# Kernel tuning notes

Measured on AMD Instinct MI355X. Metric: run time of the kernel, lower is better.

The kernel has to match this reference:

```python
import jax, jax.numpy as jnp
import numpy as np

B, T, D = 2, 2048, 512
HEADS, DIM_HEAD, MAX_LAG = 8, 64, 5
INNER = HEADS * DIM_HEAD


def setup_inputs() -> dict:
    key = jax.random.key(0)
    k0, k1, k2, k3, k4 = jax.random.split(key, 5)
    x = jax.random.normal(k0, (B, T, D), dtype=jnp.float32)
    # Linear weights stored as (in, out); torch applies x @ W.T with W (out, in).
    Wq = jax.random.normal(k1, (D, INNER), dtype=jnp.float32) * (1.0 / np.sqrt(D))
    Wk = jax.random.normal(k2, (D, INNER), dtype=jnp.float32) * (1.0 / np.sqrt(D))
    Wv = jax.random.normal(k3, (D, INNER), dtype=jnp.float32) * (1.0 / np.sqrt(D))
    Wo = jax.random.normal(k4, (INNER, D), dtype=jnp.float32) * (1.0 / np.sqrt(INNER))
    bo = jnp.zeros((D,), dtype=jnp.float32)
    # Module's init: lag_weights = log(exp(-lags/(max_lag/3))) = -lags/(max_lag/3)
    lags = jnp.arange(MAX_LAG + 1, dtype=jnp.float32)
    lag_weights = jnp.broadcast_to(-(lags / (MAX_LAG / 3.0)), (HEADS, MAX_LAG + 1)).astype(jnp.float32)
    return {"x": x, "Wq": Wq, "Wk": Wk, "Wv": Wv, "Wo": Wo, "bo": bo, "lag_weights": lag_weights}


def reference(x, Wq, Wk, Wv, Wo, bo, lag_weights):
    b, t, _ = x.shape
    h, dh = HEADS, DIM_HEAD
    scale = dh ** -0.5
    # context defaults to x (self-attention)
    q = (x @ Wq).reshape(b, t, h, dh).transpose(0, 2, 1, 3)  # b h t d
    k = (x @ Wk).reshape(b, t, h, dh).transpose(0, 2, 1, 3)
    v = (x @ Wv).reshape(b, t, h, dh).transpose(0, 2, 1, 3)
    sim = jnp.einsum('bhid,bhjd->bhij', q, k) * scale  # b h t t
    # causal mask: keep j <= i
    causal = jnp.tril(jnp.ones((t, t), dtype=bool))
    neg = -jnp.finfo(sim.dtype).max
    sim = jnp.where(causal[None, None], sim, neg)
    # learned additive time-lag bias: lag_adj[h,i,j] = softmax(lag_weights)[h, clamp(i-j,0,MAX_LAG)]
    ti = jnp.arange(t)
    time_lags = jnp.clip(ti[:, None] - ti[None, :], 0, MAX_LAG)  # t t
    lag_probs = jax.nn.softmax(lag_weights, axis=-1)  # h (L+1)
    lag_adj = lag_probs[:, time_lags]  # h t t
    sim = sim + lag_adj[None]
    attn = jax.nn.softmax(sim, axis=-1)
    out = jnp.einsum('bhij,bhjd->bhid', attn, v)
    out = out.transpose(0, 2, 1, 3).reshape(b, t, h * dh)  # b t inner
    return out @ Wo + bo  # dropout is identity at eval
```

## Files before the change

kernel.cpp:

```cpp
#include <hip/hip_runtime.h>
#include <hip/hip_bf16.h>

#define BB 2
#define TT 2048
#define DD 512
#define HH 8
#define DH 64
#define INNER 512
#define MAXLAG 5

typedef __attribute__((ext_vector_type(8))) short short8;
typedef __attribute__((ext_vector_type(4))) float floatx4;
typedef unsigned short ushort_t;

__device__ inline unsigned short f2bf(float f) {
    unsigned u = __float_as_uint(f);
    unsigned r = (u + 0x7FFFu + ((u >> 16) & 1u)) >> 16;
    return (unsigned short)r;
}
__device__ inline float bf2f(unsigned short u) {
    return __uint_as_float(((unsigned)u) << 16);
}

#define NXE (BB * TT * DD)

__global__ __launch_bounds__(256)
void cvt_kernel(const float* __restrict__ x,
                const float* __restrict__ wq, const float* __restrict__ wk,
                const float* __restrict__ wv, const float* __restrict__ wo,
                ushort_t* __restrict__ xb,
                ushort_t* __restrict__ wqt, ushort_t* __restrict__ wkt,
                ushort_t* __restrict__ wvt, ushort_t* __restrict__ wot)
{
    __shared__ float T[32][33];
    const int bid = blockIdx.x;
    if (bid < 1024) {
        int off = (bid * 256 + threadIdx.x) * 8;
        float4 a = *(const float4*)&x[off];
        float4 b = *(const float4*)&x[off + 4];
        ushort_t t[8];
        t[0] = f2bf(a.x); t[1] = f2bf(a.y); t[2] = f2bf(a.z); t[3] = f2bf(a.w);
        t[4] = f2bf(b.x); t[5] = f2bf(b.y); t[6] = f2bf(b.z); t[7] = f2bf(b.w);
        *(uint4*)&xb[off] = *(const uint4*)t;
        return;
    }
    const int r = bid - 1024;
    const int z = r >> 8;
    const int tile = r & 255;
    const float* s = (z == 0) ? wq : (z == 1) ? wk : (z == 2) ? wv : wo;
    ushort_t*    d = (z == 0) ? wqt : (z == 1) ? wkt : (z == 2) ? wvt : wot;
    const int k0 = (tile & 15) * 32;
    const int n0 = (tile >> 4) * 32;
    {
        const int kk = threadIdx.x >> 3;
        const int n4 = (threadIdx.x & 7) * 4;
        float4 v = *(const float4*)&s[(size_t)(k0 + kk) * 512 + n0 + n4];
        T[kk][n4 + 0] = v.x; T[kk][n4 + 1] = v.y;
        T[kk][n4 + 2] = v.z; T[kk][n4 + 3] = v.w;
    }
    __syncthreads();
    {
        const int nn = threadIdx.x >> 3;
        const int k4 = (threadIdx.x & 7) * 4;
        ushort4 o;
        o.x = f2bf(T[k4 + 0][nn]); o.y = f2bf(T[k4 + 1][nn]);
        o.z = f2bf(T[k4 + 2][nn]); o.w = f2bf(T[k4 + 3][nn]);
        *(ushort4*)&d[(size_t)(n0 + nn) * 512 + k0 + k4] = o;
    }
}

#define GM 64
#define GN 64
#define GK 32

template <typename OutT>
__global__ __launch_bounds__(256)
void gemm64(const ushort_t* __restrict__ A,
            const ushort_t* __restrict__ B0, const ushort_t* __restrict__ B1,
            const ushort_t* __restrict__ B2,
            OutT* __restrict__ O0, OutT* __restrict__ O1, OutT* __restrict__ O2,
            const float* __restrict__ bias, int M, int N, int K, int vtrans)
{
    const ushort_t* Bw = (blockIdx.z == 0) ? B0 : ((blockIdx.z == 1) ? B1 : B2);
    OutT*           O  = (blockIdx.z == 0) ? O0 : ((blockIdx.z == 1) ? O1 : O2);
    const int dotrans = vtrans && (blockIdx.z == 2);

    __shared__ ushort_t As[GM * GK];
    __shared__ ushort_t Bs[GN * GK];

    const int tid  = threadIdx.x;
    const int wave = tid >> 6;
    const int lane = tid & 63;
    const int quad = lane >> 4;
    const int l15  = lane & 15;
    const int wr   = wave >> 1;
    const int wc   = wave & 1;
    const int bm   = blockIdx.y * GM;
    const int bn   = blockIdx.x * GN;

    const ushort_t* ap = &A[(size_t)(bm + (tid >> 2)) * K + (tid & 3) * 8];
    const ushort_t* bp = &Bw[(size_t)(bn + (tid >> 2)) * K + (tid & 3) * 8];

    floatx4 acc[2][2];
#pragma unroll
    for (int i = 0; i < 2; ++i)
#pragma unroll
        for (int j = 0; j < 2; ++j) acc[i][j] = (floatx4){0.f, 0.f, 0.f, 0.f};

    uint4 pa = *(const uint4*)ap;
    uint4 pb = *(const uint4*)bp;

    for (int k0 = 0; k0 < K; k0 += GK) {
        __syncthreads();
        *(uint4*)&As[tid * 8] = pa;
        *(uint4*)&Bs[tid * 8] = pb;
        if (k0 + GK < K) {
            pa = *(const uint4*)(ap + k0 + GK);
            pb = *(const uint4*)(bp + k0 + GK);
        }
        __syncthreads();

        short8 af[2], bf[2];
#pragma unroll
        for (int mt = 0; mt < 2; ++mt)
            af[mt] = *(const short8*)&As[(((wr * 32 + mt * 16 + l15) << 2) + quad) * 8];
#pragma unroll
        for (int nt = 0; nt < 2; ++nt)
            bf[nt] = *(const short8*)&Bs[(((wc * 32 + nt * 16 + l15) << 2) + quad) * 8];
#pragma unroll
        for (int mt = 0; mt < 2; ++mt)
#pragma unroll
            for (int nt = 0; nt < 2; ++nt)
                acc[mt][nt] = __builtin_amdgcn_mfma_f32_16x16x32_bf16(
                    af[mt], bf[nt], acc[mt][nt], 0, 0, 0);
    }

    if (dotrans) {
#pragma unroll
        for (int mt = 0; mt < 2; ++mt) {
            const int m0 = bm + wr * 32 + mt * 16 + quad * 4;
            const int b  = m0 >> 11;
            const int t0 = m0 & 2047;
#pragma unroll
            for (int nt = 0; nt < 2; ++nt) {
                const int n = bn + wc * 32 + nt * 16 + l15;
                const int h = n >> 6, dd = n & 63;
                ushort4 o;
                o.x = f2bf(acc[mt][nt][0]); o.y = f2bf(acc[mt][nt][1]);
                o.z = f2bf(acc[mt][nt][2]); o.w = f2bf(acc[mt][nt][3]);
                *(ushort4*)&((ushort_t*)O)[((size_t)((b * 8 + h) * 64 + dd)) * 2048 + t0] = o;
            }
        }
        return;
    }

    float bv[2] = {0.f, 0.f};
    if (bias) {
#pragma unroll
        for (int nt = 0; nt < 2; ++nt)
            bv[nt] = bias[bn + wc * 32 + nt * 16 + l15];
    }
#pragma unroll
    for (int mt = 0; mt < 2; ++mt) {
#pragma unroll
        for (int nt = 0; nt < 2; ++nt) {
            const int n = bn + wc * 32 + nt * 16 + l15;
#pragma unroll
            for (int reg = 0; reg < 4; ++reg) {
                const int m = bm + wr * 32 + mt * 16 + quad * 4 + reg;
                float v = acc[mt][nt][reg] + bv[nt];
                if constexpr (sizeof(OutT) == 2)
                    O[(size_t)m * N + n] = (OutT)f2bf(v);
                else
                    O[(size_t)m * N + n] = (OutT)v;
            }
        }
    }
}

#define PAD 72
#define MFIX 10.0f

__global__ __launch_bounds__(256)
void attn_mfma(const ushort_t* __restrict__ Qg,
               const ushort_t* __restrict__ Kg,
               const ushort_t* __restrict__ Vtg,
               const float* __restrict__ lagw,
               ushort_t* __restrict__ Opart,
               float* __restrict__ Lpart)
{
    __shared__ ushort_t Ks[64 * 8 * 8];
    __shared__ ushort_t Vts[64 * 8 * 8];
    __shared__ ushort_t Pl[4][16][PAD];

    const int tid  = threadIdx.x;
    const int wave = tid >> 6;
    const int lane = tid & 63;
    const int quad = lane >> 4;
    const int l15  = lane & 15;

    const int bh = blockIdx.y;
    const int b  = bh >> 3;
    const int h  = bh & 7;
    const int c  = blockIdx.x;
    const int qt = 31 - (c >> 1);
    const int sp = c & 1;
    const int i0 = qt * 64;
    const int h1 = (qt + 1) >> 1;
    const int lo = sp ? h1 : 0;
    const int hi = sp ? (qt + 1) : h1;

    float lagb[MAXLAG + 1];
    {
        float mx = -1e30f;
#pragma unroll
        for (int l = 0; l <= MAXLAG; ++l) {
            lagb[l] = lagw[h * (MAXLAG + 1) + l];
            mx = fmaxf(mx, lagb[l]);
        }
        float s = 0.f;
#pragma unroll
        for (int l = 0; l <= MAXLAG; ++l) { lagb[l] = __expf(lagb[l] - mx); s += lagb[l]; }
        float inv = 1.f / s;
#pragma unroll
        for (int l = 0; l <= MAXLAG; ++l) lagb[l] = lagb[l] * inv - MFIX;
    }
    const float c1  = 0.125f;
    const float c2f = lagb[MAXLAG];

    short8 qf0, qf1;
    {
        const ushort_t* qbase =
            Qg + ((size_t)(b * TT + i0 + wave * 16 + l15)) * INNER + h * DH;
        qf0 = *(const short8*)(qbase + quad * 8);
        qf1 = *(const short8*)(qbase + 32 + quad * 8);
    }

    floatx4 oacc[4];
    float lsum[4] = {0.f, 0.f, 0.f, 0.f};
#pragma unroll
    for (int cb = 0; cb < 4; ++cb) oacc[cb] = (floatx4){0.f, 0.f, 0.f, 0.f};

    const int ibase = i0 + wave * 16 + quad * 4;

    const int srow = tid >> 3;
    const int sc   = tid & 7;
    const ushort_t* Kp0 = Kg + ((size_t)(b * TT) + srow) * INNER + h * DH + sc * 8;
    const ushort_t* Kp1 = Kp0 + (size_t)32 * INNER;
    const ushort_t* Vp0 = Vtg + ((size_t)(bh * 64 + srow)) * 2048 + sc * 8;
    const ushort_t* Vp1 = Vp0 + (size_t)32 * 2048;
    const int slot = (sc + srow) & 7;
    const int kdst0 = ((srow << 3) + slot) << 3;
    const int kdst1 = (((srow + 32) << 3) + slot) << 3;

    uint4 pk0, pk1, pv0, pv1;
    if (lo < hi) {
        const size_t koff = (size_t)(lo * 64) * INNER;
        pk0 = *(const uint4*)(Kp0 + koff);
        pk1 = *(const uint4*)(Kp1 + koff);
        pv0 = *(const uint4*)(Vp0 + lo * 64);
        pv1 = *(const uint4*)(Vp1 + lo * 64);
    }

    for (int kt = lo; kt < hi; ++kt) {
        __syncthreads();
        *(uint4*)&Ks[kdst0]  = pk0;
        *(uint4*)&Ks[kdst1]  = pk1;
        *(uint4*)&Vts[kdst0] = pv0;
        *(uint4*)&Vts[kdst1] = pv1;
        if (kt + 1 < hi) {
            const size_t koff = (size_t)((kt + 1) * 64) * INNER;
            pk0 = *(const uint4*)(Kp0 + koff);
            pk1 = *(const uint4*)(Kp1 + koff);
            pv0 = *(const uint4*)(Vp0 + (kt + 1) * 64);
            pv1 = *(const uint4*)(Vp1 + (kt + 1) * 64);
        }
        __syncthreads();

        const int j0 = kt * 64;

        floatx4 sacc[4];
#pragma unroll
        for (int cb = 0; cb < 4; ++cb) {
            const int key = cb * 16 + l15;
            short8 kf0 = *(const short8*)&Ks[((key << 3) + ((quad + key) & 7)) << 3];
            short8 kf1 = *(const short8*)&Ks[((key << 3) + ((quad + 4 + key) & 7)) << 3];
            floatx4 z = (floatx4){0.f, 0.f, 0.f, 0.f};
            z = __builtin_amdgcn_mfma_f32_16x16x32_bf16(qf0, kf0, z, 0, 0, 0);
            z = __builtin_amdgcn_mfma_f32_16x16x32_bf16(qf1, kf1, z, 0, 0, 0);
            sacc[cb] = z;
        }

        float p[4][4];
        if (i0 + wave * 16 - (j0 + 63) >= MAXLAG) {
#pragma unroll
            for (int cb = 0; cb < 4; ++cb)
#pragma unroll
                for (int reg = 0; reg < 4; ++reg)
                    p[cb][reg] = __expf(fmaf(sacc[cb][reg], c1, c2f));
        } else {
#pragma unroll
            for (int cb = 0; cb < 4; ++cb) {
                const int j = j0 + cb * 16 + l15;
#pragma unroll
                for (int reg = 0; reg < 4; ++reg) {
                    const int lag = (ibase + reg) - j;
                    float bias = (lag <= 0) ? lagb[0]
                               : (lag == 1) ? lagb[1]
                               : (lag == 2) ? lagb[2]
                               : (lag == 3) ? lagb[3]
                               : (lag == 4) ? lagb[4] : lagb[5];
                    float e = __expf(fmaf(sacc[cb][reg], c1, bias));
                    p[cb][reg] = (lag < 0) ? 0.f : e;
                }
            }
        }
#pragma unroll
        for (int cb = 0; cb < 4; ++cb)
#pragma unroll
            for (int reg = 0; reg < 4; ++reg)
                lsum[reg] += p[cb][reg];

#pragma unroll
        for (int cb = 0; cb < 4; ++cb)
#pragma unroll
            for (int reg = 0; reg < 4; ++reg)
                Pl[wave][quad * 4 + reg][cb * 16 + l15] = f2bf(p[cb][reg]);

        short8 pf0 = *(const short8*)&Pl[wave][l15][quad * 8];
        short8 pf1 = *(const short8*)&Pl[wave][l15][32 + quad * 8];

#pragma unroll
        for (int cb = 0; cb < 4; ++cb) {
            const int dd = cb * 16 + l15;
            short8 vf0 = *(const short8*)&Vts[((dd << 3) + ((quad + dd) & 7)) << 3];
            short8 vf1 = *(const short8*)&Vts[((dd << 3) + ((quad + 4 + dd) & 7)) << 3];
            oacc[cb] = __builtin_amdgcn_mfma_f32_16x16x32_bf16(pf0, vf0, oacc[cb], 0, 0, 0);
            oacc[cb] = __builtin_amdgcn_mfma_f32_16x16x32_bf16(pf1, vf1, oacc[cb], 0, 0, 0);
        }
    }

#pragma unroll
    for (int reg = 0; reg < 4; ++reg) {
        lsum[reg] += __shfl_xor(lsum[reg], 1);
        lsum[reg] += __shfl_xor(lsum[reg], 2);
        lsum[reg] += __shfl_xor(lsum[reg], 4);
        lsum[reg] += __shfl_xor(lsum[reg], 8);
    }

#pragma unroll
    for (int reg = 0; reg < 4; ++reg) {
        const int row = ibase + reg;
        const size_t obase = ((size_t)(sp * 16 + bh) * TT + row) * 64;
#pragma unroll
        for (int cb = 0; cb < 4; ++cb)
            Opart[obase + cb * 16 + l15] = f2bf(oacc[cb][reg]);
        if (l15 == 0)
            Lpart[(size_t)(sp * 16 + bh) * TT + row] = lsum[reg];
    }
}

#define CMB_UNITS (16 * TT * 16)

__global__ __launch_bounds__(256)
void combine_kernel(const ushort_t* __restrict__ Opart,
                    const float* __restrict__ Lpart,
                    ushort_t* __restrict__ ao)
{
    int u = blockIdx.x * 256 + threadIdx.x;
    const int bh  = u >> 15;
    const int rem = u & 32767;
    const int i   = rem >> 4;
    const int d   = (rem & 15) * 4;
    const int b   = bh >> 3;
    const int h   = bh & 7;

    const size_t p0 = ((size_t)bh * TT + i) * 64 + d;
    const size_t p1 = ((size_t)(16 + bh) * TT + i) * 64 + d;
    ushort4 a0 = *(const ushort4*)&Opart[p0];
    ushort4 a1 = *(const ushort4*)&Opart[p1];
    const float l = Lpart[(size_t)bh * TT + i] + Lpart[(size_t)(16 + bh) * TT + i];
    const float inv = 1.f / l;

    ushort4 o;
    o.x = f2bf((bf2f(a0.x) + bf2f(a1.x)) * inv);
    o.y = f2bf((bf2f(a0.y) + bf2f(a1.y)) * inv);
    o.z = f2bf((bf2f(a0.z) + bf2f(a1.z)) * inv);
    o.w = f2bf((bf2f(a0.w) + bf2f(a1.w)) * inv);
    *(ushort4*)&ao[((size_t)(b * TT + i)) * INNER + h * DH + d] = o;
}

extern "C" void kernel_launch(void* const* d_in, const int* in_sizes, int n_in,
                              void* d_out, int out_size, void* d_ws, size_t ws_size,
                              hipStream_t stream)
{
    const float* x  = (const float*)d_in[0];
    const float* Wq = (const float*)d_in[1];
    const float* Wk = (const float*)d_in[2];
    const float* Wv = (const float*)d_in[3];
    const float* Wo = (const float*)d_in[4];
    const float* bo = (const float*)d_in[5];
    const float* lw = (const float*)d_in[6];
    float* out = (float*)d_out;

    const size_t SZ  = (size_t)BB * TT * INNER;
    const size_t NWE = (size_t)DD * INNER;
    ushort_t* xb    = (ushort_t*)d_ws;
    ushort_t* wqt   = xb + SZ;
    ushort_t* wkt   = wqt + NWE;
    ushort_t* wvt   = wkt + NWE;
    ushort_t* wot   = wvt + NWE;
    ushort_t* q     = wot + NWE;
    ushort_t* k     = q + SZ;
    ushort_t* vt    = k + SZ;
    ushort_t* opart = vt + SZ;
    float*    lpart = (float*)(opart + 2 * SZ);
    ushort_t* ao    = xb;

    const int M = BB * TT;

    cvt_kernel<<<2048, 256, 0, stream>>>(x, Wq, Wk, Wv, Wo,
                                         xb, wqt, wkt, wvt, wot);

    dim3 gQKV(INNER / GN, M / GM, 3);
    gemm64<ushort_t><<<gQKV, 256, 0, stream>>>(
        xb, wqt, wkt, wvt, q, k, vt, nullptr, M, INNER, DD, 1);

    dim3 gATT(64, BB * HH);
    attn_mfma<<<gATT, 256, 0, stream>>>(q, k, vt, lw, opart, lpart);

    combine_kernel<<<CMB_UNITS / 256, 256, 0, stream>>>(opart, lpart, ao);

    dim3 gPRJ(DD / GN, M / GM, 1);
    gemm64<float><<<gPRJ, 256, 0, stream>>>(
        ao, wot, wot, wot, out, out, out, bo, M, DD, INNER, 0);
}
```

Measured before the change: 139.0 us.

## Use direct global-to-LDS loads and larger fused QKV GEMM tiles

Splits the generic GEMM into a dedicated QKV kernel and a projection kernel. The QKV kernel reads one concatenated weight matrix and uses 128x64 tiles, so each thread computes more output. Both kernels replace register-staged tile copies with the global_load_lds builtin, which writes straight into shared memory. This drops the software prefetch into registers, so global loads no longer overlap compute and the loop relies on barriers and occupancy to hide latency.

```diff
diff --git a/kernel.cpp b/kernel.cpp
--- a/kernel.cpp
+++ b/kernel.cpp
@@ -22,15 +22,18 @@
     return __uint_as_float(((unsigned)u) << 16);
 }
 
-#define NXE (BB * TT * DD)
+__device__ __forceinline__ void gload16(ushort_t* lds, const ushort_t* g) {
+    __builtin_amdgcn_global_load_lds(
+        (const __attribute__((address_space(1))) void*)g,
+        (__attribute__((address_space(3))) void*)lds, 16, 0, 0);
+}
 
 __global__ __launch_bounds__(256)
 void cvt_kernel(const float* __restrict__ x,
                 const float* __restrict__ wq, const float* __restrict__ wk,
                 const float* __restrict__ wv, const float* __restrict__ wo,
                 ushort_t* __restrict__ xb,
-                ushort_t* __restrict__ wqt, ushort_t* __restrict__ wkt,
-                ushort_t* __restrict__ wvt, ushort_t* __restrict__ wot)
+                ushort_t* __restrict__ wqkvt, ushort_t* __restrict__ wot)
 {
     __shared__ float T[32][33];
     const int bid = blockIdx.x;
@@ -48,7 +51,7 @@
     const int z = r >> 8;
     const int tile = r & 255;
     const float* s = (z == 0) ? wq : (z == 1) ? wk : (z == 2) ? wv : wo;
-    ushort_t*    d = (z == 0) ? wqt : (z == 1) ? wkt : (z == 2) ? wvt : wot;
+    ushort_t*    d = (z < 3) ? (wqkvt + (size_t)z * 512 * 512) : wot;
     const int k0 = (tile & 15) * 32;
     const int n0 = (tile >> 4) * 32;
     {
@@ -69,24 +72,17 @@
     }
 }
 
-#define GM 64
-#define GN 64
-#define GK 32
-
-template <typename OutT>
+#define QM 128
+#define QN 64
+#define QKS 32
+
 __global__ __launch_bounds__(256)
-void gemm64(const ushort_t* __restrict__ A,
-            const ushort_t* __restrict__ B0, const ushort_t* __restrict__ B1,
-            const ushort_t* __restrict__ B2,
-            OutT* __restrict__ O0, OutT* __restrict__ O1, OutT* __restrict__ O2,
-            const float* __restrict__ bias, int M, int N, int K, int vtrans)
-{
-    const ushort_t* Bw = (blockIdx.z == 0) ? B0 : ((blockIdx.z == 1) ? B1 : B2);
-    OutT*           O  = (blockIdx.z == 0) ? O0 : ((blockIdx.z == 1) ? O1 : O2);
-    const int dotrans = vtrans && (blockIdx.z == 2);
-
-    __shared__ ushort_t As[GM * GK];
-    __shared__ ushort_t Bs[GN * GK];
+void gemm_qkv(const ushort_t* __restrict__ A, const ushort_t* __restrict__ Bw,
+              ushort_t* __restrict__ q, ushort_t* __restrict__ k,
+              ushort_t* __restrict__ vt)
+{
+    __shared__ ushort_t As[QM * QKS];
+    __shared__ ushort_t Bs[QN * QKS];
 
     const int tid  = threadIdx.x;
     const int wave = tid >> 6;
@@ -95,71 +91,135 @@
     const int l15  = lane & 15;
     const int wr   = wave >> 1;
     const int wc   = wave & 1;
-    const int bm   = blockIdx.y * GM;
-    const int bn   = blockIdx.x * GN;
-
-    const ushort_t* ap = &A[(size_t)(bm + (tid >> 2)) * K + (tid & 3) * 8];
-    const ushort_t* bp = &Bw[(size_t)(bn + (tid >> 2)) * K + (tid & 3) * 8];
-
-    floatx4 acc[2][2];
-#pragma unroll
-    for (int i = 0; i < 2; ++i)
+    const int bm   = blockIdx.y * QM;
+    const int bn   = blockIdx.x * QN;
+
+    const int ga0 = wave * 128 + lane;
+    const int ga1 = ga0 + 64;
+    const ushort_t* ap0 = &A[(size_t)(bm + (ga0 >> 2)) * DD + (ga0 & 3) * 8];
+    const ushort_t* ap1 = &A[(size_t)(bm + (ga1 >> 2)) * DD + (ga1 & 3) * 8];
+    const int gb = wave * 64 + lane;
+    const ushort_t* bp = &Bw[(size_t)(bn + (gb >> 2)) * DD + (gb & 3) * 8];
+    ushort_t* lA0 = &As[(size_t)(wave * 128) * 8];
+    ushort_t* lA1 = lA0 + 64 * 8;
+    ushort_t* lB  = &Bs[(size_t)(wave * 64) * 8];
+
+    floatx4 acc[4][2];
+#pragma unroll
+    for (int i = 0; i < 4; ++i)
 #pragma unroll
         for (int j = 0; j < 2; ++j) acc[i][j] = (floatx4){0.f, 0.f, 0.f, 0.f};
 
-    uint4 pa = *(const uint4*)ap;
-    uint4 pb = *(const uint4*)bp;
-
-    for (int k0 = 0; k0 < K; k0 += GK) {
-        __syncthreads();
-        *(uint4*)&As[tid * 8] = pa;
-        *(uint4*)&Bs[tid * 8] = pb;
-        if (k0 + GK < K) {
-            pa = *(const uint4*)(ap + k0 + GK);
-            pb = *(const uint4*)(bp + k0 + GK);
-        }
-        __syncthreads();
-
-        short8 af[2], bf[2];
-#pragma unroll
-        for (int mt = 0; mt < 2; ++mt)
-            af[mt] = *(const short8*)&As[(((wr * 32 + mt * 16 + l15) << 2) + quad) * 8];
+    for (int k0 = 0; k0 < DD; k0 += QKS) {
+        __syncthreads();
+        gload16(lA0, ap0 + k0);
+        gload16(lA1, ap1 + k0);
+        gload16(lB,  bp  + k0);
+        __syncthreads();
+
+        short8 af[4], bfr[2];
+#pragma unroll
+        for (int mt = 0; mt < 4; ++mt)
+            af[mt] = *(const short8*)&As[(((wr * 64 + mt * 16 + l15) << 2) + quad) * 8];
 #pragma unroll
         for (int nt = 0; nt < 2; ++nt)
-            bf[nt] = *(const short8*)&Bs[(((wc * 32 + nt * 16 + l15) << 2) + quad) * 8];
-#pragma unroll
-        for (int mt = 0; mt < 2; ++mt)
+            bfr[nt] = *(const short8*)&Bs[(((wc * 32 + nt * 16 + l15) << 2) + quad) * 8];
+#pragma unroll
+        for (int mt = 0; mt < 4; ++mt)
 #pragma unroll
             for (int nt = 0; nt < 2; ++nt)
                 acc[mt][nt] = __builtin_amdgcn_mfma_f32_16x16x32_bf16(
-                    af[mt], bf[nt], acc[mt][nt], 0, 0, 0);
-    }
-
-    if (dotrans) {
-#pragma unroll
-        for (int mt = 0; mt < 2; ++mt) {
-            const int m0 = bm + wr * 32 + mt * 16 + quad * 4;
+                    af[mt], bfr[nt], acc[mt][nt], 0, 0, 0);
+    }
+
+    const int z = bn >> 9;
+    if (z == 2) {
+#pragma unroll
+        for (int mt = 0; mt < 4; ++mt) {
+            const int m0 = bm + wr * 64 + mt * 16 + quad * 4;
             const int b  = m0 >> 11;
             const int t0 = m0 & 2047;
 #pragma unroll
             for (int nt = 0; nt < 2; ++nt) {
-                const int n = bn + wc * 32 + nt * 16 + l15;
-                const int h = n >> 6, dd = n & 63;
+                const int n  = bn + wc * 32 + nt * 16 + l15 - 1024;
+                const int h  = n >> 6, dd = n & 63;
                 ushort4 o;
                 o.x = f2bf(acc[mt][nt][0]); o.y = f2bf(acc[mt][nt][1]);
                 o.z = f2bf(acc[mt][nt][2]); o.w = f2bf(acc[mt][nt][3]);
-                *(ushort4*)&((ushort_t*)O)[((size_t)((b * 8 + h) * 64 + dd)) * 2048 + t0] = o;
+                *(ushort4*)&vt[((size_t)((b * 8 + h) * 64 + dd)) * 2048 + t0] = o;
             }
         }
         return;
     }
-
-    float bv[2] = {0.f, 0.f};
-    if (bias) {
+    ushort_t* O = (z == 0) ? q : k;
+    const int nb = bn - z * 512;
+#pragma unroll
+    for (int mt = 0; mt < 4; ++mt) {
+#pragma unroll
+        for (int nt = 0; nt < 2; ++nt) {
+            const int n = nb + wc * 32 + nt * 16 + l15;
+#pragma unroll
+            for (int reg = 0; reg < 4; ++reg) {
+                const int m = bm + wr * 64 + mt * 16 + quad * 4 + reg;
+                O[(size_t)m * 512 + n] = f2bf(acc[mt][nt][reg]);
+            }
+        }
+    }
+}
+
+__global__ __launch_bounds__(256)
+void gemm_proj(const ushort_t* __restrict__ A, const ushort_t* __restrict__ Bw,
+               float* __restrict__ O, const float* __restrict__ bias)
+{
+    __shared__ ushort_t As[64 * 32];
+    __shared__ ushort_t Bs[64 * 32];
+
+    const int tid  = threadIdx.x;
+    const int wave = tid >> 6;
+    const int lane = tid & 63;
+    const int quad = lane >> 4;
+    const int l15  = lane & 15;
+    const int wr   = wave >> 1;
+    const int wc   = wave & 1;
+    const int bm   = blockIdx.y * 64;
+    const int bn   = blockIdx.x * 64;
+
+    const ushort_t* ap = &A[(size_t)(bm + (tid >> 2)) * INNER + (tid & 3) * 8];
+    const ushort_t* bp = &Bw[(size_t)(bn + (tid >> 2)) * INNER + (tid & 3) * 8];
+    ushort_t* lA = &As[(size_t)(wave * 64) * 8];
+    ushort_t* lB = &Bs[(size_t)(wave * 64) * 8];
+
+    floatx4 acc[2][2];
+#pragma unroll
+    for (int i = 0; i < 2; ++i)
+#pragma unroll
+        for (int j = 0; j < 2; ++j) acc[i][j] = (floatx4){0.f, 0.f, 0.f, 0.f};
+
+    for (int k0 = 0; k0 < INNER; k0 += 32) {
+        __syncthreads();
+        gload16(lA, ap + k0);
+        gload16(lB, bp + k0);
+        __syncthreads();
+
+        short8 af[2], bfr[2];
+#pragma unroll
+        for (int mt = 0; mt < 2; ++mt)
+            af[mt] = *(const short8*)&As[(((wr * 32 + mt * 16 + l15) << 2) + quad) * 8];
 #pragma unroll
         for (int nt = 0; nt < 2; ++nt)
-            bv[nt] = bias[bn + wc * 32 + nt * 16 + l15];
-    }
+            bfr[nt] = *(const short8*)&Bs[(((wc * 32 + nt * 16 + l15) << 2) + quad) * 8];
+#pragma unroll
+        for (int mt = 0; mt < 2; ++mt)
+#pragma unroll
+            for (int nt = 0; nt < 2; ++nt)
+                acc[mt][nt] = __builtin_amdgcn_mfma_f32_16x16x32_bf16(
+                    af[mt], bfr[nt], acc[mt][nt], 0, 0, 0);
+    }
+
+    float bv[2];
+#pragma unroll
+    for (int nt = 0; nt < 2; ++nt)
+        bv[nt] = bias[bn + wc * 32 + nt * 16 + l15];
 #pragma unroll
     for (int mt = 0; mt < 2; ++mt) {
 #pragma unroll
@@ -168,11 +228,7 @@
 #pragma unroll
             for (int reg = 0; reg < 4; ++reg) {
                 const int m = bm + wr * 32 + mt * 16 + quad * 4 + reg;
-                float v = acc[mt][nt][reg] + bv[nt];
-                if constexpr (sizeof(OutT) == 2)
-                    O[(size_t)m * N + n] = (OutT)f2bf(v);
-                else
-                    O[(size_t)m * N + n] = (OutT)v;
+                O[(size_t)m * 512 + n] = acc[mt][nt][reg] + bv[nt];
             }
         }
     }
@@ -285,10 +341,10 @@
             const int key = cb * 16 + l15;
             short8 kf0 = *(const short8*)&Ks[((key << 3) + ((quad + key) & 7)) << 3];
             short8 kf1 = *(const short8*)&Ks[((key << 3) + ((quad + 4 + key) & 7)) << 3];
-            floatx4 z = (floatx4){0.f, 0.f, 0.f, 0.f};
-            z = __builtin_amdgcn_mfma_f32_16x16x32_bf16(qf0, kf0, z, 0, 0, 0);
-            z = __builtin_amdgcn_mfma_f32_16x16x32_bf16(qf1, kf1, z, 0, 0, 0);
-            sacc[cb] = z;
+            floatx4 zf = (floatx4){0.f, 0.f, 0.f, 0.f};
+            zf = __builtin_amdgcn_mfma_f32_16x16x32_bf16(qf0, kf0, zf, 0, 0, 0);
+            zf = __builtin_amdgcn_mfma_f32_16x16x32_bf16(qf1, kf1, zf, 0, 0, 0);
+            sacc[cb] = zf;
         }
 
         float p[4][4];
@@ -406,10 +462,8 @@
     const size_t SZ  = (size_t)BB * TT * INNER;
     const size_t NWE = (size_t)DD * INNER;
     ushort_t* xb    = (ushort_t*)d_ws;
-    ushort_t* wqt   = xb + SZ;
-    ushort_t* wkt   = wqt + NWE;
-    ushort_t* wvt   = wkt + NWE;
-    ushort_t* wot   = wvt + NWE;
+    ushort_t* wqkvt = xb + SZ;
+    ushort_t* wot   = wqkvt + 3 * NWE;
     ushort_t* q     = wot + NWE;
     ushort_t* k     = q + SZ;
     ushort_t* vt    = k + SZ;
@@ -417,21 +471,16 @@
     float*    lpart = (float*)(opart + 2 * SZ);
     ushort_t* ao    = xb;
 
-    const int M = BB * TT;
-
-    cvt_kernel<<<2048, 256, 0, stream>>>(x, Wq, Wk, Wv, Wo,
-                                         xb, wqt, wkt, wvt, wot);
-
-    dim3 gQKV(INNER / GN, M / GM, 3);
-    gemm64<ushort_t><<<gQKV, 256, 0, stream>>>(
-        xb, wqt, wkt, wvt, q, k, vt, nullptr, M, INNER, DD, 1);
+    cvt_kernel<<<2048, 256, 0, stream>>>(x, Wq, Wk, Wv, Wo, xb, wqkvt, wot);
+
+    dim3 gQKV(3 * INNER / QN, (BB * TT) / QM);
+    gemm_qkv<<<gQKV, 256, 0, stream>>>(xb, wqkvt, q, k, vt);
 
     dim3 gATT(64, BB * HH);
     attn_mfma<<<gATT, 256, 0, stream>>>(q, k, vt, lw, opart, lpart);
 
     combine_kernel<<<CMB_UNITS / 256, 256, 0, stream>>>(opart, lpart, ao);
 
-    dim3 gPRJ(DD / GN, M / GM, 1);
-    gemm64<float><<<gPRJ, 256, 0, stream>>>(
-        ao, wot, wot, wot, out, out, out, bo, M, DD, INNER, 0);
-}
+    dim3 gPRJ(DD / 64, (BB * TT) / 64);
+    gemm_proj<<<gPRJ, 256, 0, stream>>>(ao, wot, out, bo);
+}
```

Result: no change. 139.0 us (+0.0%).
